# Kernel optimization log

Measured on AMD Instinct MI355X. Metric: run time of the kernel, lower is better.

## Reference

```python
import jax, jax.numpy as jnp
from jax import lax
import numpy as np

B, C, L = 128, 12, 2048
K, G = 8, 64
_G = G // 2  # divisor = 2 since g > 1
NCP = int(np.clip(C // 2, 2, 8))  # channels summed per group
ND = int(np.log2((L - 1) / 8)) + 1  # number of dilations = 8
DILS = [2 ** i for i in range(ND)]


def setup_inputs() -> dict:
    key = jax.random.key(0)
    kx, kw, ki = jax.random.split(key, 3)
    X = jax.random.normal(kx, (B, C, L), jnp.float32)
    # Hydra weights: zero-mean, L1-normalized over the 9-tap kernel axis
    W = jax.random.normal(kw, (ND, 2, K * _G, 1, 9), jnp.float32)
    W = W - W.mean(-1, keepdims=True)
    W = W / jnp.abs(W).sum(-1, keepdims=True)
    # random channel-subset indices per (dilation, diff, group)
    I = jax.random.randint(ki, (ND, 2, _G, NCP), 0, C, dtype=jnp.int32)
    return {"X": X, "W": W, "I": I}


def _forward(X, W, I):
    Bn = X.shape[0]
    diff_X = jnp.diff(X, axis=-1)  # [B, C, L-1]
    bi = jnp.arange(Bn)[:, None, None]
    gi = jnp.arange(_G)[None, :, None]
    Zs = []
    for di in range(ND):
        d = DILS[di]
        p = (8 * d) // 2  # same padding rule as torch: floor((9-1)*d/2)
        for diff_index in range(2):
            src = X if diff_index == 0 else diff_X
            # gather channel subsets and sum them: [B, _G, L']
            inp = src[:, I[di, diff_index]].sum(2)
            # grouped dilated conv1d, 1 input channel / K output channels per group
            out = lax.conv_general_dilated(
                inp, W[di, diff_index],
                window_strides=(1,), padding=[(p, p)],
                rhs_dilation=(d,),
                dimension_numbers=("NCH", "OIH", "NCH"),
                feature_group_count=_G)
            Zc = out.reshape(Bn, _G, K, -1)  # [B, _G, K, Lout]
            max_v = Zc.max(2)                 # [B, _G, Lout]
            max_i = Zc.argmax(2)
            min_i = Zc.argmin(2)
            # scatter-add histograms over the K kernels
            count_max = jnp.zeros((Bn, _G, K), X.dtype).at[bi, gi, max_i].add(max_v)
            count_min = jnp.zeros((Bn, _G, K), X.dtype).at[bi, gi, min_i].add(
                jnp.ones_like(max_v))
            Zs.append(count_max)
            Zs.append(count_min)
    return jnp.concatenate(Zs, 1).reshape(Bn, -1)  # [B, ND*2*2*_G*K]


def reference(X, W, I):
    return _forward(X, W, I)
```

## Files before the change

### kernel.cpp

```cpp
#include <hip/hip_runtime.h>

typedef float    v2f __attribute__((ext_vector_type(2)));
typedef unsigned v2u __attribute__((ext_vector_type(2)));

constexpr int CB   = 128;
constexpr int CC   = 12;
constexpr int CL   = 2048;
constexpr int CK   = 8;
constexpr int CG   = 32;
constexpr int CNCP = 6;
constexpr int CND  = 8;
constexpr int HALO = 512;
constexpr int BUF  = HALO + CL + HALO + 16;

__global__ void transposeW(const float* __restrict__ W, float* __restrict__ Wt) {
    int t = blockIdx.x * blockDim.x + threadIdx.x;
    constexpr int total = CND * 2 * CG * CK * 9;
    if (t >= total) return;
    int j = t % 9; int r = t / 9;
    int k = r % CK; r /= CK;
    int g = r % CG; int pair = r / CG;
    Wt[(pair * CG + g) * 72 + j * 8 + k] =
        W[((pair * (CG * CK)) + g * CK + k) * 9 + j];
}

__device__ __forceinline__ float4 ld4(const float* p) { return *(const float4*)p; }

__device__ __forceinline__ v2f packidx(v2f a, unsigned code) {
    v2u u = __builtin_bit_cast(v2u, a);
    u = (u & 0xFFFFFFF8u) | code;
    return __builtin_bit_cast(v2f, u);
}
__device__ __forceinline__ int lowbits(float v) {
    return (int)(__builtin_bit_cast(unsigned, v) & 7u);
}

__global__ void __launch_bounds__(256)
hydra_fused(const float* __restrict__ X, const float* __restrict__ Wt,
            const int* __restrict__ I, float* __restrict__ out)
{
    __shared__ float inp[BUF];
    __shared__ float wavehist[4 * 16];
    __shared__ float bins[9][256];
    const int tid = threadIdx.x;
    const int blk  = blockIdx.x;
    const int x    = blk & 7;
    const int r    = blk >> 3;
    const int pair = r & 15;
    const int gq   = (r >> 4) & 3;
    const int b    = x * 16 + (r >> 6);
    const int di    = pair >> 1;
    const int diffi = pair & 1;
    const int D     = 1 << di;
    const int Lout  = CL - diffi;
    const float* __restrict__ Xb = X + (size_t)b * (CC * CL);

    for (int i = tid; i < HALO; i += 256) inp[i] = 0.f;
    for (int i = HALO + CL + tid; i < BUF; i += 256) inp[i] = 0.f;
    #pragma unroll
    for (int k2 = 0; k2 < 8; ++k2) bins[k2][tid] = 0.f;

    #pragma unroll 1
    for (int gi = 0; gi < 8; ++gi) {
        const int g = gq * 8 + gi;
        const int* __restrict__ Ig = I + (pair * CG + g) * CNCP;
        const int ch0 = Ig[0], ch1 = Ig[1], ch2 = Ig[2],
                  ch3 = Ig[3], ch4 = Ig[4], ch5 = Ig[5];
        const float* r0 = Xb + ch0 * CL; const float* r1 = Xb + ch1 * CL;
        const float* r2 = Xb + ch2 * CL; const float* r3 = Xb + ch3 * CL;
        const float* r4 = Xb + ch4 * CL; const float* r5 = Xb + ch5 * CL;

        #pragma unroll
        for (int cc = 0; cc < 2; ++cc) {
            const int pos = cc * 1024 + tid * 4;
            const float4 x0 = ld4(r0 + pos), x1 = ld4(r1 + pos), x2 = ld4(r2 + pos),
                         x3 = ld4(r3 + pos), x4 = ld4(r4 + pos), x5 = ld4(r5 + pos);
            float4 s;
            s.x = ((x0.x + x1.x) + (x2.x + x3.x)) + (x4.x + x5.x);
            s.y = ((x0.y + x1.y) + (x2.y + x3.y)) + (x4.y + x5.y);
            s.z = ((x0.z + x1.z) + (x2.z + x3.z)) + (x4.z + x5.z);
            s.w = ((x0.w + x1.w) + (x2.w + x3.w)) + (x4.w + x5.w);
            if (!diffi) {
                *(float4*)&inp[HALO + pos] = s;
            } else {
                float s4;
                if (pos + 4 < CL)
                    s4 = ((r0[pos + 4] + r1[pos + 4]) + (r2[pos + 4] + r3[pos + 4]))
                         + (r4[pos + 4] + r5[pos + 4]);
                else
                    s4 = s.w;
                const float4 d = make_float4(s.y - s.x, s.z - s.y, s.w - s.z, s4 - s.w);
                *(float4*)&inp[HALO + pos] = d;
            }
        }
        __syncthreads();

        const float* __restrict__ Wg = Wt + (pair * CG + g) * 72;
        unsigned bnpack = 0;

        #pragma unroll 1
        for (int p = 0; p < 4; ++p) {
            const int l = p * 512 + tid * 2;
            v2f a0, a1, a2, a3, a4, a5, a6, a7;

            #define FK2M(J, TV) { const float* wj = Wg + (J) * 8; \
                a0 = (v2f){wj[0], wj[0]} * TV; \
                a1 = (v2f){wj[1], wj[1]} * TV; \
                a2 = (v2f){wj[2], wj[2]} * TV; \
                a3 = (v2f){wj[3], wj[3]} * TV; \
                a4 = (v2f){wj[4], wj[4]} * TV; \
                a5 = (v2f){wj[5], wj[5]} * TV; \
                a6 = (v2f){wj[6], wj[6]} * TV; \
                a7 = (v2f){wj[7], wj[7]} * TV; }
            #define FK2(J, TV) { const float* wj = Wg + (J) * 8; \
                a0 = __builtin_elementwise_fma((v2f){wj[0], wj[0]}, TV, a0); \
                a1 = __builtin_elementwise_fma((v2f){wj[1], wj[1]}, TV, a1); \
                a2 = __builtin_elementwise_fma((v2f){wj[2], wj[2]}, TV, a2); \
                a3 = __builtin_elementwise_fma((v2f){wj[3], wj[3]}, TV, a3); \
                a4 = __builtin_elementwise_fma((v2f){wj[4], wj[4]}, TV, a4); \
                a5 = __builtin_elementwise_fma((v2f){wj[5], wj[5]}, TV, a5); \
                a6 = __builtin_elementwise_fma((v2f){wj[6], wj[6]}, TV, a6); \
                a7 = __builtin_elementwise_fma((v2f){wj[7], wj[7]}, TV, a7); }

            if (di == 0) {
                const float* base = &inp[HALO + l - 4];
                const v2f W0 = *(const v2f*)(base + 0), W1 = *(const v2f*)(base + 2),
                          W2 = *(const v2f*)(base + 4), W3 = *(const v2f*)(base + 6),
                          W4 = *(const v2f*)(base + 8);
                FK2M(0, W0)
                FK2(1, ((v2f){W0.y, W1.x}))
                FK2(2, W1)
                FK2(3, ((v2f){W1.y, W2.x}))
                FK2(4, W2)
                FK2(5, ((v2f){W2.y, W3.x}))
                FK2(6, W3)
                FK2(7, ((v2f){W3.y, W4.x}))
                FK2(8, W4)
            } else {
                const float* base = &inp[HALO + l - 4 * D];
                {
                    const v2f tv0 = *(const v2f*)(base);
                    FK2M(0, tv0)
                }
                #pragma unroll
                for (int j = 1; j < 9; ++j) {
                    const v2f tv = *(const v2f*)(base + j * D);
                    FK2(j, tv)
                }
            }
            #undef FK2
            #undef FK2M

            const v2f q0 = packidx(a0, 0), q1 = packidx(a1, 1),
                      q2 = packidx(a2, 2), q3 = packidx(a3, 3),
                      q4 = packidx(a4, 4), q5 = packidx(a5, 5),
                      q6 = packidx(a6, 6), q7 = packidx(a7, 7);

            const float mxx = fmaxf(fmaxf(fmaxf(fmaxf(q0.x, q1.x), q2.x),
                                          fmaxf(fmaxf(q3.x, q4.x), q5.x)),
                                    fmaxf(q6.x, q7.x));
            const float mxy = fmaxf(fmaxf(fmaxf(fmaxf(q0.y, q1.y), q2.y),
                                          fmaxf(fmaxf(q3.y, q4.y), q5.y)),
                                    fmaxf(q6.y, q7.y));
            const float mnx = fminf(fminf(fminf(fminf(q0.x, q1.x), q2.x),
                                          fminf(fminf(q3.x, q4.x), q5.x)),
                                    fminf(q6.x, q7.x));
            const float mny = fminf(fminf(fminf(fminf(q0.y, q1.y), q2.y),
                                          fminf(fminf(q3.y, q4.y), q5.y)),
                                    fminf(q6.y, q7.y));

            const int mi0 = lowbits(mxx), mi1 = lowbits(mxy);
            const int ni0 = lowbits(mnx), ni1 = lowbits(mny);

            float vx = mxx, vy = mxy;
            const bool v1ok = (l + 1) < Lout;
            if (!v1ok) vy = 0.f;

            const bool eq = (mi0 == mi1);
            const float vxe = eq ? (vx + vy) : vx;
            const int   mi1p = eq ? 8 : mi1;
            float* p0 = &bins[mi0][tid];
            float* p1 = &bins[mi1p][tid];
            const float o0 = *p0;
            const float o1 = *p1;
            *p0 = o0 + vxe;
            *p1 = o1 + vy;
            bnpack += (1u << (ni0 * 4)) + (v1ok ? (1u << (ni1 * 4)) : 0u);
        }

        float f0 = bins[0][tid], f1 = bins[1][tid],
              f2 = bins[2][tid], f3 = bins[3][tid],
              f4 = bins[4][tid], f5 = bins[5][tid],
              f6 = bins[6][tid], f7 = bins[7][tid];
        #pragma unroll
        for (int k2 = 0; k2 < 8; ++k2) bins[k2][tid] = 0.f;

        float h0 = (float)((bnpack >>  0) & 15), h1 = (float)((bnpack >>  4) & 15),
              h2 = (float)((bnpack >>  8) & 15), h3 = (float)((bnpack >> 12) & 15),
              h4 = (float)((bnpack >> 16) & 15), h5 = (float)((bnpack >> 20) & 15),
              h6 = (float)((bnpack >> 24) & 15), h7 = (float)((bnpack >> 28) & 15);

        const int lane = tid & 63;
        const bool l5 = (lane & 32) != 0, l4 = (lane & 16) != 0, l3 = (lane & 8) != 0;

        #define RSCAT(q, v0, v1, v2, v3, v4, v5, v6, v7)                          \
            float q;                                                              \
            {                                                                     \
                float k0 = l5 ? v4 : v0, s0 = l5 ? v0 : v4;                       \
                float k1 = l5 ? v5 : v1, s1 = l5 ? v1 : v5;                       \
                float k2 = l5 ? v6 : v2, s2 = l5 ? v2 : v6;                       \
                float k3 = l5 ? v7 : v3, s3 = l5 ? v3 : v7;                       \
                k0 += __shfl_xor(s0, 32); k1 += __shfl_xor(s1, 32);               \
                k2 += __shfl_xor(s2, 32); k3 += __shfl_xor(s3, 32);               \
                float m0 = l4 ? k2 : k0, t0 = l4 ? k0 : k2;                       \
                float m1 = l4 ? k3 : k1, t1 = l4 ? k1 : k3;                       \
                m0 += __shfl_xor(t0, 16); m1 += __shfl_xor(t1, 16);               \
                q = l3 ? m1 : m0; float u = l3 ? m0 : m1;                         \
                q += __shfl_xor(u, 8);                                            \
                q += __shfl_xor(q, 4); q += __shfl_xor(q, 2);                     \
                q += __shfl_xor(q, 1);                                            \
            }
        RSCAT(qf, f0, f1, f2, f3, f4, f5, f6, f7)
        RSCAT(qc, h0, h1, h2, h3, h4, h5, h6, h7)
        #undef RSCAT

        if ((lane & 7) == 0) {
            const int bin = (l5 ? 4 : 0) + (l4 ? 2 : 0) + (l3 ? 1 : 0);
            float* wh = wavehist + (tid >> 6) * 16;
            wh[bin]     = qf;
            wh[8 + bin] = qc;
        }
        __syncthreads();

        if (tid < 16) {
            const float s = wavehist[tid] + wavehist[16 + tid]
                          + wavehist[32 + tid] + wavehist[48 + tid];
            const int which = tid >> 3, k = tid & 7;
            out[(size_t)b * 8192 + ((pair * 2 + which) * CG + g) * CK + k] = s;
        }
    }
}

extern "C" void kernel_launch(void* const* d_in, const int* in_sizes, int n_in,
                              void* d_out, int out_size, void* d_ws, size_t ws_size,
                              hipStream_t stream)
{
    const float* X = (const float*)d_in[0];
    const float* W = (const float*)d_in[1];
    const int*   I = (const int*)d_in[2];
    float* out = (float*)d_out;
    float* Wt  = (float*)d_ws;

    transposeW<<<dim3((36864 + 255) / 256), dim3(256), 0, stream>>>(W, Wt);
    hydra_fused<<<dim3(CB * 16 * 4), dim3(256), 0, stream>>>(X, Wt, I, out);
}
```

Baseline: 426.0 us.

## Prefetch next group's first input chunk across barrier and use LDS-only barriers

Loads the channel indices and first float4 chunk of the next group's six input rows into registers before the convolution phase of the current group. This lets the global load latency overlap with compute. Replaces __syncthreads with a barrier that waits only on LDS counters, so outstanding global prefetches are not drained at the barrier. Also shrinks the bins array by removing the dummy ninth row, reorders the two bin stores so the equal-index case stays correct, and raises launch bounds to 7 waves per EU. The cost is higher register pressure, which competes with the new occupancy target.

```diff
diff --git a/kernel.cpp b/kernel.cpp
--- a/kernel.cpp
+++ b/kernel.cpp
@@ -35,13 +35,19 @@
     return (int)(__builtin_bit_cast(unsigned, v) & 7u);
 }
 
-__global__ void __launch_bounds__(256)
+__device__ __forceinline__ void barrier_lds_only() {
+    asm volatile("s_waitcnt lgkmcnt(0)" ::: "memory");
+    __builtin_amdgcn_s_barrier();
+    asm volatile("" ::: "memory");
+}
+
+__global__ void __launch_bounds__(256, 7)
 hydra_fused(const float* __restrict__ X, const float* __restrict__ Wt,
             const int* __restrict__ I, float* __restrict__ out)
 {
     __shared__ float inp[BUF];
     __shared__ float wavehist[4 * 16];
-    __shared__ float bins[9][256];
+    __shared__ float bins[8][256];
     const int tid = threadIdx.x;
     const int blk  = blockIdx.x;
     const int x    = blk & 7;
@@ -60,19 +66,46 @@
     #pragma unroll
     for (int k2 = 0; k2 < 8; ++k2) bins[k2][tid] = 0.f;
 
+    const int gbase = gq * 8;
+    int ch0, ch1, ch2, ch3, ch4, ch5;
+    {
+        const int* Ig = I + (pair * CG + gbase) * CNCP;
+        ch0 = Ig[0]; ch1 = Ig[1]; ch2 = Ig[2];
+        ch3 = Ig[3]; ch4 = Ig[4]; ch5 = Ig[5];
+    }
+    float4 pf0, pf1, pf2, pf3, pf4, pf5;
+    {
+        const int pos = tid * 4;
+        pf0 = ld4(Xb + ch0 * CL + pos); pf1 = ld4(Xb + ch1 * CL + pos);
+        pf2 = ld4(Xb + ch2 * CL + pos); pf3 = ld4(Xb + ch3 * CL + pos);
+        pf4 = ld4(Xb + ch4 * CL + pos); pf5 = ld4(Xb + ch5 * CL + pos);
+    }
+
     #pragma unroll 1
     for (int gi = 0; gi < 8; ++gi) {
-        const int g = gq * 8 + gi;
-        const int* __restrict__ Ig = I + (pair * CG + g) * CNCP;
-        const int ch0 = Ig[0], ch1 = Ig[1], ch2 = Ig[2],
-                  ch3 = Ig[3], ch4 = Ig[4], ch5 = Ig[5];
+        const int g = gbase + gi;
         const float* r0 = Xb + ch0 * CL; const float* r1 = Xb + ch1 * CL;
         const float* r2 = Xb + ch2 * CL; const float* r3 = Xb + ch3 * CL;
         const float* r4 = Xb + ch4 * CL; const float* r5 = Xb + ch5 * CL;
 
-        #pragma unroll
-        for (int cc = 0; cc < 2; ++cc) {
-            const int pos = cc * 1024 + tid * 4;
+        {
+            const int pos = tid * 4;
+            float4 s;
+            s.x = ((pf0.x + pf1.x) + (pf2.x + pf3.x)) + (pf4.x + pf5.x);
+            s.y = ((pf0.y + pf1.y) + (pf2.y + pf3.y)) + (pf4.y + pf5.y);
+            s.z = ((pf0.z + pf1.z) + (pf2.z + pf3.z)) + (pf4.z + pf5.z);
+            s.w = ((pf0.w + pf1.w) + (pf2.w + pf3.w)) + (pf4.w + pf5.w);
+            if (!diffi) {
+                *(float4*)&inp[HALO + pos] = s;
+            } else {
+                const float s4 = ((r0[pos + 4] + r1[pos + 4]) + (r2[pos + 4] + r3[pos + 4]))
+                               + (r4[pos + 4] + r5[pos + 4]);
+                const float4 d = make_float4(s.y - s.x, s.z - s.y, s.w - s.z, s4 - s.w);
+                *(float4*)&inp[HALO + pos] = d;
+            }
+        }
+        {
+            const int pos = 1024 + tid * 4;
             const float4 x0 = ld4(r0 + pos), x1 = ld4(r1 + pos), x2 = ld4(r2 + pos),
                          x3 = ld4(r3 + pos), x4 = ld4(r4 + pos), x5 = ld4(r5 + pos);
             float4 s;
@@ -93,7 +126,16 @@
                 *(float4*)&inp[HALO + pos] = d;
             }
         }
-        __syncthreads();
+        if (gi < 7) {
+            const int* Ig = I + (pair * CG + (g + 1)) * CNCP;
+            ch0 = Ig[0]; ch1 = Ig[1]; ch2 = Ig[2];
+            ch3 = Ig[3]; ch4 = Ig[4]; ch5 = Ig[5];
+            const int pos = tid * 4;
+            pf0 = ld4(Xb + ch0 * CL + pos); pf1 = ld4(Xb + ch1 * CL + pos);
+            pf2 = ld4(Xb + ch2 * CL + pos); pf3 = ld4(Xb + ch3 * CL + pos);
+            pf4 = ld4(Xb + ch4 * CL + pos); pf5 = ld4(Xb + ch5 * CL + pos);
+        }
+        barrier_lds_only();
 
         const float* __restrict__ Wg = Wt + (pair * CG + g) * 72;
         unsigned bnpack = 0;
@@ -178,13 +220,12 @@
 
             const bool eq = (mi0 == mi1);
             const float vxe = eq ? (vx + vy) : vx;
-            const int   mi1p = eq ? 8 : mi1;
             float* p0 = &bins[mi0][tid];
-            float* p1 = &bins[mi1p][tid];
+            float* p1 = &bins[mi1][tid];
             const float o0 = *p0;
             const float o1 = *p1;
+            *p1 = o1 + vy;
             *p0 = o0 + vxe;
-            *p1 = o1 + vy;
             bnpack += (1u << (ni0 * 4)) + (v1ok ? (1u << (ni1 * 4)) : 0u);
         }
 
@@ -230,7 +271,7 @@
             wh[bin]     = qf;
             wh[8 + bin] = qc;
         }
-        __syncthreads();
+        barrier_lds_only();
 
         if (tid < 16) {
             const float s = wavehist[tid] + wavehist[16 + tid]
```

Result: slower. 544.7 us (+27.9%).

## Add a dedicated staging wave with double-buffered shared input to overlap loads

Applied to the files above, without the earlier changes.

Adds a fifth wavefront per block that gathers and sums the channel subset for the next group into a second shared-memory buffer while the four compute waves convolve the current group. This is meant to hide the global-load latency of staging behind the convolution and histogram work. In exchange, shared memory per block roughly doubles, there is an extra wave per block, and the staging work is serialized onto one wave. That may reduce occupancy and make the stager the bottleneck.

```diff
diff --git a/kernel.cpp b/kernel.cpp
--- a/kernel.cpp
+++ b/kernel.cpp
@@ -11,7 +11,7 @@
 constexpr int CNCP = 6;
 constexpr int CND  = 8;
 constexpr int HALO = 512;
-constexpr int BUF  = HALO + CL + HALO + 16;
+constexpr int BUF  = HALO + CL + HALO;
 
 __global__ void transposeW(const float* __restrict__ W, float* __restrict__ Wt) {
     int t = blockIdx.x * blockDim.x + threadIdx.x;
@@ -35,13 +35,14 @@
     return (int)(__builtin_bit_cast(unsigned, v) & 7u);
 }
 
-__global__ void __launch_bounds__(256)
+__global__ void __launch_bounds__(320)
 hydra_fused(const float* __restrict__ X, const float* __restrict__ Wt,
             const int* __restrict__ I, float* __restrict__ out)
 {
-    __shared__ float inp[BUF];
-    __shared__ float wavehist[4 * 16];
+    __shared__ __align__(16) float inpA[BUF];
+    __shared__ __align__(16) float inpB[BUF];
     __shared__ float bins[9][256];
+    __shared__ float wavehist[2][64];
     const int tid = threadIdx.x;
     const int blk  = blockIdx.x;
     const int x    = blk & 7;
@@ -55,186 +56,204 @@
     const int Lout  = CL - diffi;
     const float* __restrict__ Xb = X + (size_t)b * (CC * CL);
 
-    for (int i = tid; i < HALO; i += 256) inp[i] = 0.f;
-    for (int i = HALO + CL + tid; i < BUF; i += 256) inp[i] = 0.f;
-    #pragma unroll
-    for (int k2 = 0; k2 < 8; ++k2) bins[k2][tid] = 0.f;
-
-    #pragma unroll 1
-    for (int gi = 0; gi < 8; ++gi) {
-        const int g = gq * 8 + gi;
-        const int* __restrict__ Ig = I + (pair * CG + g) * CNCP;
-        const int ch0 = Ig[0], ch1 = Ig[1], ch2 = Ig[2],
-                  ch3 = Ig[3], ch4 = Ig[4], ch5 = Ig[5];
-        const float* r0 = Xb + ch0 * CL; const float* r1 = Xb + ch1 * CL;
-        const float* r2 = Xb + ch2 * CL; const float* r3 = Xb + ch3 * CL;
-        const float* r4 = Xb + ch4 * CL; const float* r5 = Xb + ch5 * CL;
-
+    for (int i = tid; i < HALO; i += 320) { inpA[i] = 0.f; inpB[i] = 0.f; }
+    for (int i = HALO + CL + tid; i < BUF; i += 320) { inpA[i] = 0.f; inpB[i] = 0.f; }
+    if (tid < 256) {
         #pragma unroll
-        for (int cc = 0; cc < 2; ++cc) {
-            const int pos = cc * 1024 + tid * 4;
-            const float4 x0 = ld4(r0 + pos), x1 = ld4(r1 + pos), x2 = ld4(r2 + pos),
-                         x3 = ld4(r3 + pos), x4 = ld4(r4 + pos), x5 = ld4(r5 + pos);
+        for (int k2 = 0; k2 < 8; ++k2) bins[k2][tid] = 0.f;
+    }
+
+    const int  gbase  = gq * 8;
+    const bool stager = (tid >= 256);
+    const int  slane  = tid & 63;
+
+    auto stage = [&](float* dst, int gg) {
+        const int* Igs = I + (pair * CG + gg) * CNCP;
+        const int c0 = Igs[0], c1 = Igs[1], c2 = Igs[2],
+                  c3 = Igs[3], c4 = Igs[4], c5 = Igs[5];
+        const float* s0 = Xb + c0 * CL; const float* s1 = Xb + c1 * CL;
+        const float* s2 = Xb + c2 * CL; const float* s3 = Xb + c3 * CL;
+        const float* s4p = Xb + c4 * CL; const float* s5 = Xb + c5 * CL;
+        #pragma unroll 2
+        for (int it = 0; it < 8; ++it) {
+            const int pos = it * 256 + slane * 4;
+            const float4 x0 = ld4(s0 + pos), x1 = ld4(s1 + pos), x2 = ld4(s2 + pos),
+                         x3 = ld4(s3 + pos), x4 = ld4(s4p + pos), x5 = ld4(s5 + pos);
             float4 s;
             s.x = ((x0.x + x1.x) + (x2.x + x3.x)) + (x4.x + x5.x);
             s.y = ((x0.y + x1.y) + (x2.y + x3.y)) + (x4.y + x5.y);
             s.z = ((x0.z + x1.z) + (x2.z + x3.z)) + (x4.z + x5.z);
             s.w = ((x0.w + x1.w) + (x2.w + x3.w)) + (x4.w + x5.w);
             if (!diffi) {
-                *(float4*)&inp[HALO + pos] = s;
+                *(float4*)&dst[HALO + pos] = s;
             } else {
                 float s4;
                 if (pos + 4 < CL)
-                    s4 = ((r0[pos + 4] + r1[pos + 4]) + (r2[pos + 4] + r3[pos + 4]))
-                         + (r4[pos + 4] + r5[pos + 4]);
+                    s4 = ((s0[pos + 4] + s1[pos + 4]) + (s2[pos + 4] + s3[pos + 4]))
+                         + (s4p[pos + 4] + s5[pos + 4]);
                 else
                     s4 = s.w;
                 const float4 d = make_float4(s.y - s.x, s.z - s.y, s.w - s.z, s4 - s.w);
-                *(float4*)&inp[HALO + pos] = d;
+                *(float4*)&dst[HALO + pos] = d;
+            }
+        }
+    };
+
+    if (stager) stage(inpA, gbase);
+    __syncthreads();
+
+    #pragma unroll 1
+    for (int gi = 0; gi < 8; ++gi) {
+        const int g   = gbase + gi;
+        const int cur = gi & 1;
+        float* curbuf = cur ? inpB : inpA;
+        float* nxtbuf = cur ? inpA : inpB;
+
+        if (stager) {
+            if (gi < 7) stage(nxtbuf, g + 1);
+        } else {
+            const float* inp = curbuf;
+            const float* __restrict__ Wg = Wt + (pair * CG + g) * 72;
+            unsigned bnpack = 0;
+
+            #pragma unroll 1
+            for (int p = 0; p < 4; ++p) {
+                const int l = p * 512 + tid * 2;
+                v2f a0, a1, a2, a3, a4, a5, a6, a7;
+
+                #define FK2M(J, TV) { const float* wj = Wg + (J) * 8; \
+                    a0 = (v2f){wj[0], wj[0]} * TV; \
+                    a1 = (v2f){wj[1], wj[1]} * TV; \
+                    a2 = (v2f){wj[2], wj[2]} * TV; \
+                    a3 = (v2f){wj[3], wj[3]} * TV; \
+                    a4 = (v2f){wj[4], wj[4]} * TV; \
+                    a5 = (v2f){wj[5], wj[5]} * TV; \
+                    a6 = (v2f){wj[6], wj[6]} * TV; \
+                    a7 = (v2f){wj[7], wj[7]} * TV; }
+                #define FK2(J, TV) { const float* wj = Wg + (J) * 8; \
+                    a0 = __builtin_elementwise_fma((v2f){wj[0], wj[0]}, TV, a0); \
+                    a1 = __builtin_elementwise_fma((v2f){wj[1], wj[1]}, TV, a1); \
+                    a2 = __builtin_elementwise_fma((v2f){wj[2], wj[2]}, TV, a2); \
+                    a3 = __builtin_elementwise_fma((v2f){wj[3], wj[3]}, TV, a3); \
+                    a4 = __builtin_elementwise_fma((v2f){wj[4], wj[4]}, TV, a4); \
+                    a5 = __builtin_elementwise_fma((v2f){wj[5], wj[5]}, TV, a5); \
+                    a6 = __builtin_elementwise_fma((v2f){wj[6], wj[6]}, TV, a6); \
+                    a7 = __builtin_elementwise_fma((v2f){wj[7], wj[7]}, TV, a7); }
+
+                if (di == 0) {
+                    const float* base = &inp[HALO + l - 4];
+                    const v2f W0 = *(const v2f*)(base + 0), W1 = *(const v2f*)(base + 2),
+                              W2 = *(const v2f*)(base + 4), W3 = *(const v2f*)(base + 6),
+                              W4 = *(const v2f*)(base + 8);
+                    FK2M(0, W0)
+                    FK2(1, ((v2f){W0.y, W1.x}))
+                    FK2(2, W1)
+                    FK2(3, ((v2f){W1.y, W2.x}))
+                    FK2(4, W2)
+                    FK2(5, ((v2f){W2.y, W3.x}))
+                    FK2(6, W3)
+                    FK2(7, ((v2f){W3.y, W4.x}))
+                    FK2(8, W4)
+                } else {
+                    const float* base = &inp[HALO + l - 4 * D];
+                    {
+                        const v2f tv0 = *(const v2f*)(base);
+                        FK2M(0, tv0)
+                    }
+                    #pragma unroll
+                    for (int j = 1; j < 9; ++j) {
+                        const v2f tv = *(const v2f*)(base + j * D);
+                        FK2(j, tv)
+                    }
+                }
+                #undef FK2
+                #undef FK2M
+
+                const v2f q0 = packidx(a0, 0), q1 = packidx(a1, 1),
+                          q2 = packidx(a2, 2), q3 = packidx(a3, 3),
+                          q4 = packidx(a4, 4), q5 = packidx(a5, 5),
+                          q6 = packidx(a6, 6), q7 = packidx(a7, 7);
+
+                const float mxx = fmaxf(fmaxf(fmaxf(fmaxf(q0.x, q1.x), q2.x),
+                                              fmaxf(fmaxf(q3.x, q4.x), q5.x)),
+                                        fmaxf(q6.x, q7.x));
+                const float mxy = fmaxf(fmaxf(fmaxf(fmaxf(q0.y, q1.y), q2.y),
+                                              fmaxf(fmaxf(q3.y, q4.y), q5.y)),
+                                        fmaxf(q6.y, q7.y));
+                const float mnx = fminf(fminf(fminf(fminf(q0.x, q1.x), q2.x),
+                                              fminf(fminf(q3.x, q4.x), q5.x)),
+                                        fminf(q6.x, q7.x));
+                const float mny = fminf(fminf(fminf(fminf(q0.y, q1.y), q2.y),
+                                              fminf(fminf(q3.y, q4.y), q5.y)),
+                                        fminf(q6.y, q7.y));
+
+                const int mi0 = lowbits(mxx), mi1 = lowbits(mxy);
+                const int ni0 = lowbits(mnx), ni1 = lowbits(mny);
+
+                float vx = mxx, vy = mxy;
+                const bool v1ok = (l + 1) < Lout;
+                if (!v1ok) vy = 0.f;
+
+                const bool eq = (mi0 == mi1);
+                const float vxe = eq ? (vx + vy) : vx;
+                const int   mi1p = eq ? 8 : mi1;
+                float* p0 = &bins[mi0][tid];
+                float* p1 = &bins[mi1p][tid];
+                const float o0 = *p0;
+                const float o1 = *p1;
+                *p0 = o0 + vxe;
+                *p1 = o1 + vy;
+                bnpack += (1u << (ni0 * 4)) + (v1ok ? (1u << (ni1 * 4)) : 0u);
+            }
+
+            float f0 = bins[0][tid], f1 = bins[1][tid],
+                  f2 = bins[2][tid], f3 = bins[3][tid],
+                  f4 = bins[4][tid], f5 = bins[5][tid],
+                  f6 = bins[6][tid], f7 = bins[7][tid];
+            #pragma unroll
+            for (int k2 = 0; k2 < 8; ++k2) bins[k2][tid] = 0.f;
+
+            float h0 = (float)((bnpack >>  0) & 15), h1 = (float)((bnpack >>  4) & 15),
+                  h2 = (float)((bnpack >>  8) & 15), h3 = (float)((bnpack >> 12) & 15),
+                  h4 = (float)((bnpack >> 16) & 15), h5 = (float)((bnpack >> 20) & 15),
+                  h6 = (float)((bnpack >> 24) & 15), h7 = (float)((bnpack >> 28) & 15);
+
+            const int lane = tid & 63;
+            const bool l5 = (lane & 32) != 0, l4 = (lane & 16) != 0, l3 = (lane & 8) != 0;
+
+            #define RSCAT(q, v0, v1, v2, v3, v4, v5, v6, v7)                          \
+                float q;                                                              \
+                {                                                                     \
+                    float k0 = l5 ? v4 : v0, s0 = l5 ? v0 : v4;                       \
+                    float k1 = l5 ? v5 : v1, s1 = l5 ? v1 : v5;                       \
+                    float k2 = l5 ? v6 : v2, s2 = l5 ? v2 : v6;                       \
+                    float k3 = l5 ? v7 : v3, s3 = l5 ? v3 : v7;                       \
+                    k0 += __shfl_xor(s0, 32); k1 += __shfl_xor(s1, 32);               \
+                    k2 += __shfl_xor(s2, 32); k3 += __shfl_xor(s3, 32);               \
+                    float m0 = l4 ? k2 : k0, t0 = l4 ? k0 : k2;                       \
+                    float m1 = l4 ? k3 : k1, t1 = l4 ? k1 : k3;                       \
+                    m0 += __shfl_xor(t0, 16); m1 += __shfl_xor(t1, 16);               \
+                    q = l3 ? m1 : m0; float u = l3 ? m0 : m1;                         \
+                    q += __shfl_xor(u, 8);                                            \
+                    q += __shfl_xor(q, 4); q += __shfl_xor(q, 2);                     \
+                    q += __shfl_xor(q, 1);                                            \
+                }
+            RSCAT(qf, f0, f1, f2, f3, f4, f5, f6, f7)
+            RSCAT(qc, h0, h1, h2, h3, h4, h5, h6, h7)
+            #undef RSCAT
+
+            if ((lane & 7) == 0) {
+                const int bin = (l5 ? 4 : 0) + (l4 ? 2 : 0) + (l3 ? 1 : 0);
+                float* wh = wavehist[cur] + (tid >> 6) * 16;
+                wh[bin]     = qf;
+                wh[8 + bin] = qc;
             }
         }
         __syncthreads();
 
-        const float* __restrict__ Wg = Wt + (pair * CG + g) * 72;
-        unsigned bnpack = 0;
-
-        #pragma unroll 1
-        for (int p = 0; p < 4; ++p) {
-            const int l = p * 512 + tid * 2;
-            v2f a0, a1, a2, a3, a4, a5, a6, a7;
-
-            #define FK2M(J, TV) { const float* wj = Wg + (J) * 8; \
-                a0 = (v2f){wj[0], wj[0]} * TV; \
-                a1 = (v2f){wj[1], wj[1]} * TV; \
-                a2 = (v2f){wj[2], wj[2]} * TV; \
-                a3 = (v2f){wj[3], wj[3]} * TV; \
-                a4 = (v2f){wj[4], wj[4]} * TV; \
-                a5 = (v2f){wj[5], wj[5]} * TV; \
-                a6 = (v2f){wj[6], wj[6]} * TV; \
-                a7 = (v2f){wj[7], wj[7]} * TV; }
-            #define FK2(J, TV) { const float* wj = Wg + (J) * 8; \
-                a0 = __builtin_elementwise_fma((v2f){wj[0], wj[0]}, TV, a0); \
-                a1 = __builtin_elementwise_fma((v2f){wj[1], wj[1]}, TV, a1); \
-                a2 = __builtin_elementwise_fma((v2f){wj[2], wj[2]}, TV, a2); \
-                a3 = __builtin_elementwise_fma((v2f){wj[3], wj[3]}, TV, a3); \
-                a4 = __builtin_elementwise_fma((v2f){wj[4], wj[4]}, TV, a4); \
-                a5 = __builtin_elementwise_fma((v2f){wj[5], wj[5]}, TV, a5); \
-                a6 = __builtin_elementwise_fma((v2f){wj[6], wj[6]}, TV, a6); \
-                a7 = __builtin_elementwise_fma((v2f){wj[7], wj[7]}, TV, a7); }
-
-            if (di == 0) {
-                const float* base = &inp[HALO + l - 4];
-                const v2f W0 = *(const v2f*)(base + 0), W1 = *(const v2f*)(base + 2),
-                          W2 = *(const v2f*)(base + 4), W3 = *(const v2f*)(base + 6),
-                          W4 = *(const v2f*)(base + 8);
-                FK2M(0, W0)
-                FK2(1, ((v2f){W0.y, W1.x}))
-                FK2(2, W1)
-                FK2(3, ((v2f){W1.y, W2.x}))
-                FK2(4, W2)
-                FK2(5, ((v2f){W2.y, W3.x}))
-                FK2(6, W3)
-                FK2(7, ((v2f){W3.y, W4.x}))
-                FK2(8, W4)
-            } else {
-                const float* base = &inp[HALO + l - 4 * D];
-                {
-                    const v2f tv0 = *(const v2f*)(base);
-                    FK2M(0, tv0)
-                }
-                #pragma unroll
-                for (int j = 1; j < 9; ++j) {
-                    const v2f tv = *(const v2f*)(base + j * D);
-                    FK2(j, tv)
-                }
-            }
-            #undef FK2
-            #undef FK2M
-
-            const v2f q0 = packidx(a0, 0), q1 = packidx(a1, 1),
-                      q2 = packidx(a2, 2), q3 = packidx(a3, 3),
-                      q4 = packidx(a4, 4), q5 = packidx(a5, 5),
-                      q6 = packidx(a6, 6), q7 = packidx(a7, 7);
-
-            const float mxx = fmaxf(fmaxf(fmaxf(fmaxf(q0.x, q1.x), q2.x),
-                                          fmaxf(fmaxf(q3.x, q4.x), q5.x)),
-                                    fmaxf(q6.x, q7.x));
-            const float mxy = fmaxf(fmaxf(fmaxf(fmaxf(q0.y, q1.y), q2.y),
-                                          fmaxf(fmaxf(q3.y, q4.y), q5.y)),
-                                    fmaxf(q6.y, q7.y));
-            const float mnx = fminf(fminf(fminf(fminf(q0.x, q1.x), q2.x),
-                                          fminf(fminf(q3.x, q4.x), q5.x)),
-                                    fminf(q6.x, q7.x));
-            const float mny = fminf(fminf(fminf(fminf(q0.y, q1.y), q2.y),
-                                          fminf(fminf(q3.y, q4.y), q5.y)),
-                                    fminf(q6.y, q7.y));
-
-            const int mi0 = lowbits(mxx), mi1 = lowbits(mxy);
-            const int ni0 = lowbits(mnx), ni1 = lowbits(mny);
-
-            float vx = mxx, vy = mxy;
-            const bool v1ok = (l + 1) < Lout;
-            if (!v1ok) vy = 0.f;
-
-            const bool eq = (mi0 == mi1);
-            const float vxe = eq ? (vx + vy) : vx;
-            const int   mi1p = eq ? 8 : mi1;
-            float* p0 = &bins[mi0][tid];
-            float* p1 = &bins[mi1p][tid];
-            const float o0 = *p0;
-            const float o1 = *p1;
-            *p0 = o0 + vxe;
-            *p1 = o1 + vy;
-            bnpack += (1u << (ni0 * 4)) + (v1ok ? (1u << (ni1 * 4)) : 0u);
-        }
-
-        float f0 = bins[0][tid], f1 = bins[1][tid],
-              f2 = bins[2][tid], f3 = bins[3][tid],
-              f4 = bins[4][tid], f5 = bins[5][tid],
-              f6 = bins[6][tid], f7 = bins[7][tid];
-        #pragma unroll
-        for (int k2 = 0; k2 < 8; ++k2) bins[k2][tid] = 0.f;
-
-        float h0 = (float)((bnpack >>  0) & 15), h1 = (float)((bnpack >>  4) & 15),
-              h2 = (float)((bnpack >>  8) & 15), h3 = (float)((bnpack >> 12) & 15),
-              h4 = (float)((bnpack >> 16) & 15), h5 = (float)((bnpack >> 20) & 15),
-              h6 = (float)((bnpack >> 24) & 15), h7 = (float)((bnpack >> 28) & 15);
-
-        const int lane = tid & 63;
-        const bool l5 = (lane & 32) != 0, l4 = (lane & 16) != 0, l3 = (lane & 8) != 0;
-
-        #define RSCAT(q, v0, v1, v2, v3, v4, v5, v6, v7)                          \
-            float q;                                                              \
-            {                                                                     \
-                float k0 = l5 ? v4 : v0, s0 = l5 ? v0 : v4;                       \
-                float k1 = l5 ? v5 : v1, s1 = l5 ? v1 : v5;                       \
-                float k2 = l5 ? v6 : v2, s2 = l5 ? v2 : v6;                       \
-                float k3 = l5 ? v7 : v3, s3 = l5 ? v3 : v7;                       \
-                k0 += __shfl_xor(s0, 32); k1 += __shfl_xor(s1, 32);               \
-                k2 += __shfl_xor(s2, 32); k3 += __shfl_xor(s3, 32);               \
-                float m0 = l4 ? k2 : k0, t0 = l4 ? k0 : k2;                       \
-                float m1 = l4 ? k3 : k1, t1 = l4 ? k1 : k3;                       \
-                m0 += __shfl_xor(t0, 16); m1 += __shfl_xor(t1, 16);               \
-                q = l3 ? m1 : m0; float u = l3 ? m0 : m1;                         \
-                q += __shfl_xor(u, 8);                                            \
-                q += __shfl_xor(q, 4); q += __shfl_xor(q, 2);                     \
-                q += __shfl_xor(q, 1);                                            \
-            }
-        RSCAT(qf, f0, f1, f2, f3, f4, f5, f6, f7)
-        RSCAT(qc, h0, h1, h2, h3, h4, h5, h6, h7)
-        #undef RSCAT
-
-        if ((lane & 7) == 0) {
-            const int bin = (l5 ? 4 : 0) + (l4 ? 2 : 0) + (l3 ? 1 : 0);
-            float* wh = wavehist + (tid >> 6) * 16;
-            wh[bin]     = qf;
-            wh[8 + bin] = qc;
-        }
-        __syncthreads();
-
         if (tid < 16) {
-            const float s = wavehist[tid] + wavehist[16 + tid]
-                          + wavehist[32 + tid] + wavehist[48 + tid];
+            const float* wh = wavehist[cur];
+            const float s = wh[tid] + wh[16 + tid] + wh[32 + tid] + wh[48 + tid];
             const int which = tid >> 3, k = tid & 7;
             out[(size_t)b * 8192 + ((pair * 2 + which) * CG + g) * CK + k] = s;
         }
@@ -252,5 +271,5 @@
     float* Wt  = (float*)d_ws;
 
     transposeW<<<dim3((36864 + 255) / 256), dim3(256), 0, stream>>>(W, Wt);
-    hydra_fused<<<dim3(CB * 16 * 4), dim3(256), 0, stream>>>(X, Wt, I, out);
-}
+    hydra_fused<<<dim3(CB * 16 * 4), dim3(320), 0, stream>>>(X, Wt, I, out);
+}
```

Result: slower. 754.3 us (+77.1%).
